# Kernel tuning notes

Measured on AMD Instinct MI355X. Metric: run time of the kernel, lower is better.

## Reference

```python
import jax, jax.numpy as jnp
import numpy as np

T, B, IN, H = 1024, 128, 256, 512


def setup_inputs() -> dict:
    key = jax.random.key(0)
    k1, k2, k3, k4, k5 = jax.random.split(key, 5)
    s = 1.0 / np.sqrt(H)  # PyTorch LSTM init scale
    return {
        "x": jax.random.normal(k1, (T, B, IN), dtype=jnp.float32),
        "W_ih": jax.random.normal(k2, (4 * H, IN), dtype=jnp.float32) * s,
        "W_hh": jax.random.normal(k3, (4 * H, H), dtype=jnp.float32) * s,
        "b_ih": jax.random.normal(k4, (4 * H,), dtype=jnp.float32) * s,
        "b_hh": jax.random.normal(k5, (4 * H,), dtype=jnp.float32) * s,
    }


def reference(x, W_ih, W_hh, b_ih, b_hh):
    # Single-layer unidirectional LSTM scanned over the full sequence.
    # PyTorch gate order within the 4H dim: i, f, g, o.
    b = b_ih + b_hh
    Wx = jnp.einsum('tbi,gi->tbg', x, W_ih) + b  # precompute input projection [T,B,4H]

    def step(carry, zx):
        h, c = carry
        z = zx + h @ W_hh.T  # [B, 4H]
        i, f, g, o = jnp.split(z, 4, axis=-1)
        i = jax.nn.sigmoid(i)
        f = jax.nn.sigmoid(f)
        g = jnp.tanh(g)
        o = jax.nn.sigmoid(o)
        c = f * c + i * g
        h = o * jnp.tanh(c)
        return (h, c), None

    h0 = jnp.zeros((B, H), dtype=x.dtype)
    c0 = jnp.zeros((B, H), dtype=x.dtype)
    (h, c), _ = jax.lax.scan(step, (h0, c0), Wx)
    # Original returns the LAST step's output plus (h_n, c_n); with 1 layer output == h_n.
    output = h[None]          # [1, B, H]
    h_n = h[None]             # [num_layers=1, B, H]
    c_n = c[None]
    return (output, h_n, c_n)
```

## Files before the change

### kernel.cpp

```cpp
#include <hip/hip_runtime.h>
#include <hip/hip_bf16.h>

typedef __attribute__((ext_vector_type(8)))  short short8;
typedef __attribute__((ext_vector_type(16))) float f32x16;
typedef __attribute__((ext_vector_type(4)))  unsigned int uint4v;

#define TSTEPS 1024
#define BATCH  128
#define NIN    256
#define NHID   512
#define GM     4
#define GHB    16
#define MBLK   32
#define NHB    32
#define LDSW   776

__device__ __forceinline__ unsigned short f2bf(float f) {
  unsigned int u = __builtin_bit_cast(unsigned int, f);
  u += 0x7fffu + ((u >> 16) & 1u);
  return (unsigned short)(u >> 16);
}

__device__ __forceinline__ unsigned long long pack4(float a, float b, float c, float d) {
  return (unsigned long long)f2bf(a)
       | ((unsigned long long)f2bf(b) << 16)
       | ((unsigned long long)f2bf(c) << 32)
       | ((unsigned long long)f2bf(d) << 48);
}

__device__ __forceinline__ float sigf(float x) {
  return 1.0f / (1.0f + __expf(-x));
}
__device__ __forceinline__ float tanh_fast(float x) {
  x = fminf(fmaxf(x, -15.0f), 15.0f);
  float e = __expf(2.0f * x);
  return (e - 1.0f) / (e + 1.0f);
}

__global__ void init_ws_kernel(unsigned long long* hbuf, unsigned int* flags) {
  int idx = blockIdx.x * blockDim.x + threadIdx.x;
  if (idx < 16384) hbuf[idx] = 0ull;
  if (idx < 2048) flags[idx] = 0u;
}

__global__ __launch_bounds__(256, 1) void lstm_persistent(
    const float* __restrict__ x,
    const float* __restrict__ Wih,
    const float* __restrict__ Whh,
    const float* __restrict__ bih,
    const float* __restrict__ bhh,
    float* __restrict__ out,
    unsigned long long* __restrict__ hbuf,
    unsigned int* __restrict__ flags)
{
  const int tid  = threadIdx.x;
  const int lane = tid & 63;
  const int wv   = tid >> 6;
  const int gm   = blockIdx.x & (GM - 1);
  const int gh   = blockIdx.x >> 2;
  const int m0   = gm * MBLK;
  const int hc0  = gh * NHB;

  __shared__ short in_lds[MBLK][LDSW];
  __shared__ float z_lds[4][32][36];

  const int ncol = lane & 31;
  const int kg   = (lane >> 5) * 8;
  const int gate = ncol >> 3;
  const int wrow = gate * NHID + hc0 + wv * 8 + (ncol & 7);

  short8 bfrag[48];
#pragma unroll
  for (int kb = 0; kb < 48; ++kb) {
    const float* src = (kb < 16)
        ? (Wih + (size_t)wrow * NIN  + (kb * 16 + kg))
        : (Whh + (size_t)wrow * NHID + (kb * 16 + kg - NIN));
    float4 f0 = *(const float4*)src;
    float4 f1 = *(const float4*)(src + 4);
    short8 b;
    b[0] = (short)f2bf(f0.x); b[1] = (short)f2bf(f0.y);
    b[2] = (short)f2bf(f0.z); b[3] = (short)f2bf(f0.w);
    b[4] = (short)f2bf(f1.x); b[5] = (short)f2bf(f1.y);
    b[6] = (short)f2bf(f1.z); b[7] = (short)f2bf(f1.w);
    bfrag[kb] = b;
  }

  const float bias_c = bih[wrow] + bhh[wrow];

  const int grow = tid >> 3;
  const int c4   = (tid & 7) * 4;
  float creg[4] = {0.0f, 0.0f, 0.0f, 0.0f};

  const short* abase = &in_lds[lane & 31][kg];
  unsigned int* fgrp   = flags + gm * (GHB * 32);
  unsigned int* myflag = fgrp + gh * 32;

#define XLOAD(i, v) { int u = tid + 256 * (i); \
    v = *(const float4*)(xt + (size_t)(u >> 6) * NIN + (u & 63) * 4); }
#define XPACK(i, v) { int u = tid + 256 * (i); \
    *(unsigned long long*)&in_lds[u >> 6][(u & 63) * 4] = pack4(v.x, v.y, v.z, v.w); }

  f32x16 a0, a1, a2, a3;
  float4 xv0, xv1, xv2, xv3, xv4, xv5, xv6, xv7;

  {
    const float* xt = x + (size_t)m0 * NIN;
    XLOAD(0, xv0) XLOAD(1, xv1) XLOAD(2, xv2) XLOAD(3, xv3)
    XLOAD(4, xv4) XLOAD(5, xv5) XLOAD(6, xv6) XLOAD(7, xv7)
    XPACK(0, xv0) XPACK(1, xv1) XPACK(2, xv2) XPACK(3, xv3)
    XPACK(4, xv4) XPACK(5, xv5) XPACK(6, xv6) XPACK(7, xv7)
  }
  __syncthreads();
  a0 = (f32x16)bias_c;
  a1 = (f32x16)0.0f; a2 = (f32x16)0.0f; a3 = (f32x16)0.0f;
#pragma unroll
  for (int kb = 0; kb < 16; kb += 4) {
    short8 v0 = *(const short8*)(abase + (kb + 0) * 16);
    a0 = __builtin_amdgcn_mfma_f32_32x32x16_bf16(v0, bfrag[kb + 0], a0, 0, 0, 0);
    short8 v1 = *(const short8*)(abase + (kb + 1) * 16);
    a1 = __builtin_amdgcn_mfma_f32_32x32x16_bf16(v1, bfrag[kb + 1], a1, 0, 0, 0);
    short8 v2 = *(const short8*)(abase + (kb + 2) * 16);
    a2 = __builtin_amdgcn_mfma_f32_32x32x16_bf16(v2, bfrag[kb + 2], a2, 0, 0, 0);
    short8 v3 = *(const short8*)(abase + (kb + 3) * 16);
    a3 = __builtin_amdgcn_mfma_f32_32x32x16_bf16(v3, bfrag[kb + 3], a3, 0, 0, 0);
  }

  for (int t = 0; t < TSTEPS; ++t) {
    {
      const unsigned int* fp = fgrp + (lane & (GHB - 1)) * 32;
      unsigned int v = __hip_atomic_load(fp, __ATOMIC_RELAXED, __HIP_MEMORY_SCOPE_AGENT);
      while (!__all((int)(v >= (unsigned int)t))) {
        __builtin_amdgcn_s_sleep(1);
        v = __hip_atomic_load(fp, __ATOMIC_RELAXED, __HIP_MEMORY_SCOPE_AGENT);
      }
    }

    {
      const char* hbase = (const char*)(hbuf + (size_t)(t & 1) * 16384 + (size_t)m0 * 128);
      uint4v hv0, hv1, hv2, hv3, hv4, hv5, hv6, hv7;
      const char* p = hbase + tid * 16;
      asm volatile("global_load_dwordx4 %0, %1, off sc0 sc1" : "=v"(hv0) : "v"(p + 0 * 4096));
      asm volatile("global_load_dwordx4 %0, %1, off sc0 sc1" : "=v"(hv1) : "v"(p + 1 * 4096));
      asm volatile("global_load_dwordx4 %0, %1, off sc0 sc1" : "=v"(hv2) : "v"(p + 2 * 4096));
      asm volatile("global_load_dwordx4 %0, %1, off sc0 sc1" : "=v"(hv3) : "v"(p + 3 * 4096));
      asm volatile("global_load_dwordx4 %0, %1, off sc0 sc1" : "=v"(hv4) : "v"(p + 4 * 4096));
      asm volatile("global_load_dwordx4 %0, %1, off sc0 sc1" : "=v"(hv5) : "v"(p + 5 * 4096));
      asm volatile("global_load_dwordx4 %0, %1, off sc0 sc1" : "=v"(hv6) : "v"(p + 6 * 4096));
      asm volatile("global_load_dwordx4 %0, %1, off sc0 sc1" : "=v"(hv7) : "v"(p + 7 * 4096));
      asm volatile("s_waitcnt vmcnt(0)" ::: "memory");
      __builtin_amdgcn_sched_barrier(0);
#pragma unroll
      for (int i = 0; i < 8; ++i) {
        int u  = tid + 256 * i;
        int r  = u >> 6;
        int cu = (u & 63) * 8;
        uint4v v = (i == 0) ? hv0 : (i == 1) ? hv1 : (i == 2) ? hv2 : (i == 3) ? hv3
                 : (i == 4) ? hv4 : (i == 5) ? hv5 : (i == 6) ? hv6 : hv7;
        *(uint4v*)&in_lds[r][NIN + cu] = v;
      }
    }
    __syncthreads();

#pragma unroll
    for (int kb = 16; kb < 48; kb += 4) {
      short8 v0 = *(const short8*)(abase + (kb + 0) * 16);
      a0 = __builtin_amdgcn_mfma_f32_32x32x16_bf16(v0, bfrag[kb + 0], a0, 0, 0, 0);
      short8 v1 = *(const short8*)(abase + (kb + 1) * 16);
      a1 = __builtin_amdgcn_mfma_f32_32x32x16_bf16(v1, bfrag[kb + 1], a1, 0, 0, 0);
      short8 v2 = *(const short8*)(abase + (kb + 2) * 16);
      a2 = __builtin_amdgcn_mfma_f32_32x32x16_bf16(v2, bfrag[kb + 2], a2, 0, 0, 0);
      short8 v3 = *(const short8*)(abase + (kb + 3) * 16);
      a3 = __builtin_amdgcn_mfma_f32_32x32x16_bf16(v3, bfrag[kb + 3], a3, 0, 0, 0);
    }
    {
      f32x16 acc = (a0 + a1) + (a2 + a3);
#pragma unroll
      for (int r = 0; r < 16; ++r) {
        int zr = (r & 3) + 8 * (r >> 2) + 4 * (lane >> 5);
        z_lds[wv][zr][ncol] = acc[r];
      }
    }
    __syncthreads();

    if (t < TSTEPS - 1) {
      const float* xt = x + ((size_t)(t + 1) * BATCH + m0) * NIN;
      XLOAD(0, xv0) XLOAD(1, xv1) XLOAD(2, xv2) XLOAD(3, xv3)
      XLOAD(4, xv4) XLOAD(5, xv5) XLOAD(6, xv6) XLOAD(7, xv7)
    }

    {
      const int wz = c4 >> 3;
      const int cc = c4 & 7;
      float hnv[4];
#pragma unroll
      for (int u = 0; u < 4; ++u) {
        float zi = z_lds[wz][grow][ 0 + cc + u];
        float zf = z_lds[wz][grow][ 8 + cc + u];
        float zg = z_lds[wz][grow][16 + cc + u];
        float zo = z_lds[wz][grow][24 + cc + u];
        float iv = sigf(zi);
        float fv = sigf(zf);
        float gv = tanh_fast(zg);
        float ov = sigf(zo);
        float cn = fv * creg[u] + iv * gv;
        creg[u] = cn;
        hnv[u] = ov * tanh_fast(cn);
      }
      if (t == TSTEPS - 1) {
        size_t o = (size_t)(m0 + grow) * NHID + hc0 + c4;
#pragma unroll
        for (int u = 0; u < 4; ++u) {
          out[o + u]          = hnv[u];
          out[65536 + o + u]  = hnv[u];
          out[131072 + o + u] = creg[u];
        }
      } else {
        unsigned long long hp = pack4(hnv[0], hnv[1], hnv[2], hnv[3]);
        size_t hoff = (size_t)((t + 1) & 1) * 16384
                    + (size_t)(m0 + grow) * 128 + (hc0 + c4) / 4;
        __hip_atomic_store(hbuf + hoff, hp, __ATOMIC_RELAXED, __HIP_MEMORY_SCOPE_AGENT);
      }
    }

    __syncthreads();

    if (t < TSTEPS - 1) {
      if (tid == 0) {
        __hip_atomic_store(myflag, (unsigned int)(t + 1),
                           __ATOMIC_RELAXED, __HIP_MEMORY_SCOPE_AGENT);
      }
      XPACK(0, xv0) XPACK(1, xv1) XPACK(2, xv2) XPACK(3, xv3)
      XPACK(4, xv4) XPACK(5, xv5) XPACK(6, xv6) XPACK(7, xv7)
      __syncthreads();
      a0 = (f32x16)bias_c;
      a1 = (f32x16)0.0f; a2 = (f32x16)0.0f; a3 = (f32x16)0.0f;
#pragma unroll
      for (int kb = 0; kb < 16; kb += 4) {
        short8 v0 = *(const short8*)(abase + (kb + 0) * 16);
        a0 = __builtin_amdgcn_mfma_f32_32x32x16_bf16(v0, bfrag[kb + 0], a0, 0, 0, 0);
        short8 v1 = *(const short8*)(abase + (kb + 1) * 16);
        a1 = __builtin_amdgcn_mfma_f32_32x32x16_bf16(v1, bfrag[kb + 1], a1, 0, 0, 0);
        short8 v2 = *(const short8*)(abase + (kb + 2) * 16);
        a2 = __builtin_amdgcn_mfma_f32_32x32x16_bf16(v2, bfrag[kb + 2], a2, 0, 0, 0);
        short8 v3 = *(const short8*)(abase + (kb + 3) * 16);
        a3 = __builtin_amdgcn_mfma_f32_32x32x16_bf16(v3, bfrag[kb + 3], a3, 0, 0, 0);
      }
    }
  }
#undef XLOAD
#undef XPACK
}

extern "C" void kernel_launch(void* const* d_in, const int* in_sizes, int n_in,
                              void* d_out, int out_size, void* d_ws, size_t ws_size,
                              hipStream_t stream) {
  const float* x   = (const float*)d_in[0];
  const float* Wih = (const float*)d_in[1];
  const float* Whh = (const float*)d_in[2];
  const float* bih = (const float*)d_in[3];
  const float* bhh = (const float*)d_in[4];
  float* out = (float*)d_out;

  unsigned long long* hbuf = (unsigned long long*)d_ws;
  unsigned int* flags = (unsigned int*)((char*)d_ws + 262144);

  hipLaunchKernelGGL(init_ws_kernel, dim3(64), dim3(256), 0, stream, hbuf, flags);
  hipLaunchKernelGGL(lstm_persistent, dim3(64), dim3(256), 0, stream,
                     x, Wih, Whh, bih, bhh, out, hbuf, flags);
}
```

Before: 3.752 ms.

## Use per-wave flags, double-buffered x/h LDS with XOR swizzle, fewer barriers

Each wave now runs its own gate nonlinearity on its z tile and publishes a per-wave flag, which removes two block-wide barriers per step. Consumers spin on 64 flags without sleeping. The x and h tiles get separate double-buffered, XOR-swizzled LDS buffers, so the x projection for the next step can be packed without waiting on a barrier, and x is prefetched two steps ahead. This is meant to shorten the serial critical path of each timestep. The cost is more flag polling traffic, and the correctness of the LDS reuse now depends on subtle ordering.

```diff
diff --git a/kernel.cpp b/kernel.cpp
--- a/kernel.cpp
+++ b/kernel.cpp
@@ -13,7 +13,8 @@
 #define GHB    16
 #define MBLK   32
 #define NHB    32
-#define LDSW   776
+#define XSTR   264
+#define HSTR   520
 
 __device__ __forceinline__ unsigned short f2bf(float f) {
   unsigned int u = __builtin_bit_cast(unsigned int, f);
@@ -40,8 +41,12 @@
 __global__ void init_ws_kernel(unsigned long long* hbuf, unsigned int* flags) {
   int idx = blockIdx.x * blockDim.x + threadIdx.x;
   if (idx < 16384) hbuf[idx] = 0ull;
-  if (idx < 2048) flags[idx] = 0u;
-}
+  if (idx < 8192) flags[idx] = 0u;
+}
+
+#define MFMA(va, fb, acc) \
+  acc = __builtin_amdgcn_mfma_f32_32x32x16_bf16(va, fb, acc, 0, 0, 0)
+#define AFRAG(base, kb) (*(const short8*)((base) + ((((kb) ^ x2) << 4) + (h5 << 3))))
 
 __global__ __launch_bounds__(256, 1) void lstm_persistent(
     const float* __restrict__ x,
@@ -61,8 +66,9 @@
   const int m0   = gm * MBLK;
   const int hc0  = gh * NHB;
 
-  __shared__ short in_lds[MBLK][LDSW];
-  __shared__ float z_lds[4][32][36];
+  __shared__ short x_lds[2][MBLK][XSTR];
+  __shared__ short h_lds[2][MBLK][HSTR];
+  __shared__ float z_lds[4][MBLK][36];
 
   const int ncol = lane & 31;
   const int kg   = (lane >> 5) * 8;
@@ -84,21 +90,23 @@
     b[6] = (short)f2bf(f1.z); b[7] = (short)f2bf(f1.w);
     bfrag[kb] = b;
   }
-
   const float bias_c = bih[wrow] + bhh[wrow];
 
-  const int grow = tid >> 3;
-  const int c4   = (tid & 7) * 4;
+  const int h5   = lane >> 5;
+  const int x2   = (lane >> 3) & 3;
+  const int arow = lane & 31;
+  const int grow = lane >> 1;
+  const int gcol = (lane & 1) * 4;
   float creg[4] = {0.0f, 0.0f, 0.0f, 0.0f};
 
-  const short* abase = &in_lds[lane & 31][kg];
-  unsigned int* fgrp   = flags + gm * (GHB * 32);
-  unsigned int* myflag = fgrp + gh * 32;
+  unsigned int* fgrp   = flags + gm * (64 * 32);
+  unsigned int* myflag = fgrp + (gh * 4 + wv) * 32;
 
 #define XLOAD(i, v) { int u = tid + 256 * (i); \
     v = *(const float4*)(xt + (size_t)(u >> 6) * NIN + (u & 63) * 4); }
-#define XPACK(i, v) { int u = tid + 256 * (i); \
-    *(unsigned long long*)&in_lds[u >> 6][(u & 63) * 4] = pack4(v.x, v.y, v.z, v.w); }
+#define XPACK(s, i, v) { int u = tid + 256 * (i); int r = u >> 6; int hc = u & 63; \
+    int off = ((((hc >> 1) ^ (((r >> 3) & 3) << 1))) << 3) + ((hc & 1) << 2); \
+    *(unsigned long long*)&x_lds[s][r][off] = pack4(v.x, v.y, v.z, v.w); }
 
   f32x16 a0, a1, a2, a3;
   float4 xv0, xv1, xv2, xv3, xv4, xv5, xv6, xv7;
@@ -107,38 +115,43 @@
     const float* xt = x + (size_t)m0 * NIN;
     XLOAD(0, xv0) XLOAD(1, xv1) XLOAD(2, xv2) XLOAD(3, xv3)
     XLOAD(4, xv4) XLOAD(5, xv5) XLOAD(6, xv6) XLOAD(7, xv7)
-    XPACK(0, xv0) XPACK(1, xv1) XPACK(2, xv2) XPACK(3, xv3)
-    XPACK(4, xv4) XPACK(5, xv5) XPACK(6, xv6) XPACK(7, xv7)
+    XPACK(0, 0, xv0) XPACK(0, 1, xv1) XPACK(0, 2, xv2) XPACK(0, 3, xv3)
+    XPACK(0, 4, xv4) XPACK(0, 5, xv5) XPACK(0, 6, xv6) XPACK(0, 7, xv7)
   }
   __syncthreads();
+  {
+    const float* xt = x + ((size_t)BATCH + m0) * NIN;
+    XLOAD(0, xv0) XLOAD(1, xv1) XLOAD(2, xv2) XLOAD(3, xv3)
+    XLOAD(4, xv4) XLOAD(5, xv5) XLOAD(6, xv6) XLOAD(7, xv7)
+  }
   a0 = (f32x16)bias_c;
   a1 = (f32x16)0.0f; a2 = (f32x16)0.0f; a3 = (f32x16)0.0f;
-#pragma unroll
-  for (int kb = 0; kb < 16; kb += 4) {
-    short8 v0 = *(const short8*)(abase + (kb + 0) * 16);
-    a0 = __builtin_amdgcn_mfma_f32_32x32x16_bf16(v0, bfrag[kb + 0], a0, 0, 0, 0);
-    short8 v1 = *(const short8*)(abase + (kb + 1) * 16);
-    a1 = __builtin_amdgcn_mfma_f32_32x32x16_bf16(v1, bfrag[kb + 1], a1, 0, 0, 0);
-    short8 v2 = *(const short8*)(abase + (kb + 2) * 16);
-    a2 = __builtin_amdgcn_mfma_f32_32x32x16_bf16(v2, bfrag[kb + 2], a2, 0, 0, 0);
-    short8 v3 = *(const short8*)(abase + (kb + 3) * 16);
-    a3 = __builtin_amdgcn_mfma_f32_32x32x16_bf16(v3, bfrag[kb + 3], a3, 0, 0, 0);
-  }
+  {
+    const short* xrow = &x_lds[0][arow][0];
+#pragma unroll
+    for (int kb = 0; kb < 16; kb += 4) {
+      MFMA(AFRAG(xrow, kb + 0), bfrag[kb + 0], a0);
+      MFMA(AFRAG(xrow, kb + 1), bfrag[kb + 1], a1);
+      MFMA(AFRAG(xrow, kb + 2), bfrag[kb + 2], a2);
+      MFMA(AFRAG(xrow, kb + 3), bfrag[kb + 3], a3);
+    }
+  }
+  XPACK(1, 0, xv0) XPACK(1, 1, xv1) XPACK(1, 2, xv2) XPACK(1, 3, xv3)
+  XPACK(1, 4, xv4) XPACK(1, 5, xv5) XPACK(1, 6, xv6) XPACK(1, 7, xv7)
 
   for (int t = 0; t < TSTEPS; ++t) {
-    {
-      const unsigned int* fp = fgrp + (lane & (GHB - 1)) * 32;
+    if (t > 0) {
+      const unsigned int* fp = fgrp + lane * 32;
       unsigned int v = __hip_atomic_load(fp, __ATOMIC_RELAXED, __HIP_MEMORY_SCOPE_AGENT);
       while (!__all((int)(v >= (unsigned int)t))) {
-        __builtin_amdgcn_s_sleep(1);
         v = __hip_atomic_load(fp, __ATOMIC_RELAXED, __HIP_MEMORY_SCOPE_AGENT);
       }
     }
 
     {
-      const char* hbase = (const char*)(hbuf + (size_t)(t & 1) * 16384 + (size_t)m0 * 128);
+      const char* p =
+          (const char*)(hbuf + (size_t)(t & 1) * 16384 + (size_t)m0 * 128) + tid * 16;
       uint4v hv0, hv1, hv2, hv3, hv4, hv5, hv6, hv7;
-      const char* p = hbase + tid * 16;
       asm volatile("global_load_dwordx4 %0, %1, off sc0 sc1" : "=v"(hv0) : "v"(p + 0 * 4096));
       asm volatile("global_load_dwordx4 %0, %1, off sc0 sc1" : "=v"(hv1) : "v"(p + 1 * 4096));
       asm volatile("global_load_dwordx4 %0, %1, off sc0 sc1" : "=v"(hv2) : "v"(p + 2 * 4096));
@@ -151,99 +164,95 @@
       __builtin_amdgcn_sched_barrier(0);
 #pragma unroll
       for (int i = 0; i < 8; ++i) {
-        int u  = tid + 256 * i;
-        int r  = u >> 6;
-        int cu = (u & 63) * 8;
+        int r   = wv + 4 * i;
+        int c16 = lane ^ (((r >> 3) & 3) << 1);
         uint4v v = (i == 0) ? hv0 : (i == 1) ? hv1 : (i == 2) ? hv2 : (i == 3) ? hv3
                  : (i == 4) ? hv4 : (i == 5) ? hv5 : (i == 6) ? hv6 : hv7;
-        *(uint4v*)&in_lds[r][NIN + cu] = v;
+        *(uint4v*)&h_lds[t & 1][r][c16 << 3] = v;
       }
     }
     __syncthreads();
 
-#pragma unroll
-    for (int kb = 16; kb < 48; kb += 4) {
-      short8 v0 = *(const short8*)(abase + (kb + 0) * 16);
-      a0 = __builtin_amdgcn_mfma_f32_32x32x16_bf16(v0, bfrag[kb + 0], a0, 0, 0, 0);
-      short8 v1 = *(const short8*)(abase + (kb + 1) * 16);
-      a1 = __builtin_amdgcn_mfma_f32_32x32x16_bf16(v1, bfrag[kb + 1], a1, 0, 0, 0);
-      short8 v2 = *(const short8*)(abase + (kb + 2) * 16);
-      a2 = __builtin_amdgcn_mfma_f32_32x32x16_bf16(v2, bfrag[kb + 2], a2, 0, 0, 0);
-      short8 v3 = *(const short8*)(abase + (kb + 3) * 16);
-      a3 = __builtin_amdgcn_mfma_f32_32x32x16_bf16(v3, bfrag[kb + 3], a3, 0, 0, 0);
-    }
+    if (t + 2 < TSTEPS) {
+      const float* xt = x + ((size_t)(t + 2) * BATCH + m0) * NIN;
+      XLOAD(0, xv0) XLOAD(1, xv1) XLOAD(2, xv2) XLOAD(3, xv3)
+      XLOAD(4, xv4) XLOAD(5, xv5) XLOAD(6, xv6) XLOAD(7, xv7)
+    }
+
+    {
+      const short* hrow = &h_lds[t & 1][arow][0];
+#pragma unroll
+      for (int kb = 0; kb < 32; kb += 4) {
+        MFMA(AFRAG(hrow, kb + 0), bfrag[16 + kb + 0], a0);
+        MFMA(AFRAG(hrow, kb + 1), bfrag[16 + kb + 1], a1);
+        MFMA(AFRAG(hrow, kb + 2), bfrag[16 + kb + 2], a2);
+        MFMA(AFRAG(hrow, kb + 3), bfrag[16 + kb + 3], a3);
+      }
+    }
+
     {
       f32x16 acc = (a0 + a1) + (a2 + a3);
 #pragma unroll
       for (int r = 0; r < 16; ++r) {
-        int zr = (r & 3) + 8 * (r >> 2) + 4 * (lane >> 5);
+        int zr = (r & 3) + 8 * (r >> 2) + 4 * h5;
         z_lds[wv][zr][ncol] = acc[r];
       }
-    }
-    __syncthreads();
-
-    if (t < TSTEPS - 1) {
-      const float* xt = x + ((size_t)(t + 1) * BATCH + m0) * NIN;
-      XLOAD(0, xv0) XLOAD(1, xv1) XLOAD(2, xv2) XLOAD(3, xv3)
-      XLOAD(4, xv4) XLOAD(5, xv5) XLOAD(6, xv6) XLOAD(7, xv7)
-    }
-
-    {
-      const int wz = c4 >> 3;
-      const int cc = c4 & 7;
+      asm volatile("s_waitcnt lgkmcnt(0)" ::: "memory");
+      const float* zrow = &z_lds[wv][grow][0];
+      float4 vi = *(const float4*)&zrow[ 0 + gcol];
+      float4 vf = *(const float4*)&zrow[ 8 + gcol];
+      float4 vg = *(const float4*)&zrow[16 + gcol];
+      float4 vo = *(const float4*)&zrow[24 + gcol];
+      float zi[4] = {vi.x, vi.y, vi.z, vi.w};
+      float zf[4] = {vf.x, vf.y, vf.z, vf.w};
+      float zg[4] = {vg.x, vg.y, vg.z, vg.w};
+      float zo[4] = {vo.x, vo.y, vo.z, vo.w};
       float hnv[4];
 #pragma unroll
       for (int u = 0; u < 4; ++u) {
-        float zi = z_lds[wz][grow][ 0 + cc + u];
-        float zf = z_lds[wz][grow][ 8 + cc + u];
-        float zg = z_lds[wz][grow][16 + cc + u];
-        float zo = z_lds[wz][grow][24 + cc + u];
-        float iv = sigf(zi);
-        float fv = sigf(zf);
-        float gv = tanh_fast(zg);
-        float ov = sigf(zo);
+        float iv = sigf(zi[u]);
+        float fv = sigf(zf[u]);
+        float gv = tanh_fast(zg[u]);
+        float ov = sigf(zo[u]);
         float cn = fv * creg[u] + iv * gv;
         creg[u] = cn;
         hnv[u] = ov * tanh_fast(cn);
       }
       if (t == TSTEPS - 1) {
-        size_t o = (size_t)(m0 + grow) * NHID + hc0 + c4;
-#pragma unroll
-        for (int u = 0; u < 4; ++u) {
-          out[o + u]          = hnv[u];
-          out[65536 + o + u]  = hnv[u];
-          out[131072 + o + u] = creg[u];
-        }
+        size_t o = (size_t)(m0 + grow) * NHID + hc0 + wv * 8 + gcol;
+        float4 hq; hq.x = hnv[0]; hq.y = hnv[1]; hq.z = hnv[2]; hq.w = hnv[3];
+        float4 cq; cq.x = creg[0]; cq.y = creg[1]; cq.z = creg[2]; cq.w = creg[3];
+        *(float4*)&out[o]          = hq;
+        *(float4*)&out[65536 + o]  = hq;
+        *(float4*)&out[131072 + o] = cq;
       } else {
         unsigned long long hp = pack4(hnv[0], hnv[1], hnv[2], hnv[3]);
         size_t hoff = (size_t)((t + 1) & 1) * 16384
-                    + (size_t)(m0 + grow) * 128 + (hc0 + c4) / 4;
+                    + (size_t)(m0 + grow) * 128 + (hc0 + wv * 8 + gcol) / 4;
         __hip_atomic_store(hbuf + hoff, hp, __ATOMIC_RELAXED, __HIP_MEMORY_SCOPE_AGENT);
-      }
-    }
-
-    __syncthreads();
+        asm volatile("s_waitcnt vmcnt(0)" ::: "memory");
+        if (lane == 0) {
+          __hip_atomic_store(myflag, (unsigned int)(t + 1),
+                             __ATOMIC_RELAXED, __HIP_MEMORY_SCOPE_AGENT);
+        }
+      }
+    }
+
+    if (t + 2 < TSTEPS) {
+      XPACK(t & 1, 0, xv0) XPACK(t & 1, 1, xv1) XPACK(t & 1, 2, xv2) XPACK(t & 1, 3, xv3)
+      XPACK(t & 1, 4, xv4) XPACK(t & 1, 5, xv5) XPACK(t & 1, 6, xv6) XPACK(t & 1, 7, xv7)
+    }
 
     if (t < TSTEPS - 1) {
-      if (tid == 0) {
-        __hip_atomic_store(myflag, (unsigned int)(t + 1),
-                           __ATOMIC_RELAXED, __HIP_MEMORY_SCOPE_AGENT);
-      }
-      XPACK(0, xv0) XPACK(1, xv1) XPACK(2, xv2) XPACK(3, xv3)
-      XPACK(4, xv4) XPACK(5, xv5) XPACK(6, xv6) XPACK(7, xv7)
-      __syncthreads();
       a0 = (f32x16)bias_c;
       a1 = (f32x16)0.0f; a2 = (f32x16)0.0f; a3 = (f32x16)0.0f;
+      const short* xrow = &x_lds[(t + 1) & 1][arow][0];
 #pragma unroll
       for (int kb = 0; kb < 16; kb += 4) {
-        short8 v0 = *(const short8*)(abase + (kb + 0) * 16);
-        a0 = __builtin_amdgcn_mfma_f32_32x32x16_bf16(v0, bfrag[kb + 0], a0, 0, 0, 0);
-        short8 v1 = *(const short8*)(abase + (kb + 1) * 16);
-        a1 = __builtin_amdgcn_mfma_f32_32x32x16_bf16(v1, bfrag[kb + 1], a1, 0, 0, 0);
-        short8 v2 = *(const short8*)(abase + (kb + 2) * 16);
-        a2 = __builtin_amdgcn_mfma_f32_32x32x16_bf16(v2, bfrag[kb + 2], a2, 0, 0, 0);
-        short8 v3 = *(const short8*)(abase + (kb + 3) * 16);
-        a3 = __builtin_amdgcn_mfma_f32_32x32x16_bf16(v3, bfrag[kb + 3], a3, 0, 0, 0);
+        MFMA(AFRAG(xrow, kb + 0), bfrag[kb + 0], a0);
+        MFMA(AFRAG(xrow, kb + 1), bfrag[kb + 1], a1);
+        MFMA(AFRAG(xrow, kb + 2), bfrag[kb + 2], a2);
+        MFMA(AFRAG(xrow, kb + 3), bfrag[kb + 3], a3);
       }
     }
   }
```

After: 4.105 ms. +9.4%, slower.
